# Kernel optimization log

Hardware: AMD Instinct MI355X
Metric: run time of the kernel (lower is better)

Reference implementation:

```python
import jax, jax.numpy as jnp
import numpy as np

ENC_VTH = 0.999      # ENCODER_REGULAR_VTH
CDECAY = 0.5         # NEURON_CDECAY
VDECAY = 0.75        # NEURON_VDECAY
VTH = 0.5            # NEURON_VTH
WIN = 0.5            # SPIKE_PSEUDO_GRAD_WINDOW
T = 5                # spike_ts

# --- pseudo-gradient spike functions ---
@jax.custom_vjp
def enc_spike(v):
    return (v > ENC_VTH).astype(v.dtype)
def _enc_fwd(v):
    return enc_spike(v), None
def _enc_bwd(_, g):
    return (g,)  # straight-through
enc_spike.defvjp(_enc_fwd, _enc_bwd)

@jax.custom_vjp
def rect_spike(v):
    return (v > VTH).astype(v.dtype)
def _rect_fwd(v):
    return rect_spike(v), v
def _rect_bwd(v, g):
    return (g * (jnp.abs(v - VTH) < WIN).astype(g.dtype),)
rect_spike.defvjp(_rect_fwd, _rect_bwd)


def setup_inputs() -> dict:
    key = jax.random.key(0)
    ks = jax.random.split(key, 8)
    B, obs_dim, en_pop, act_dim, de_pop = 8192, 128, 10, 8, 10
    H1, H2 = 256, 256
    N = obs_dim * en_pop           # 1280
    O = act_dim * de_pop           # 80
    obs = jax.random.normal(ks[0], (B, obs_dim), jnp.float32)
    # encoder mean: linspace over mean_range per population, std constant 0.15
    mean_row = jnp.linspace(-3.0, 3.0, en_pop, dtype=jnp.float32)
    enc_mean = jnp.broadcast_to(mean_row, (1, obs_dim, en_pop)).astype(jnp.float32)
    enc_std = jnp.full((1, obs_dim, en_pop), 0.15, jnp.float32)
    W1 = jax.random.normal(ks[1], (H1, N), jnp.float32) / np.sqrt(N)
    b1 = jnp.zeros((H1,), jnp.float32)
    W2 = jax.random.normal(ks[2], (H2, H1), jnp.float32) / np.sqrt(H1)
    b2 = jnp.zeros((H2,), jnp.float32)
    Wo = jax.random.normal(ks[3], (O, H2), jnp.float32) / np.sqrt(H2)
    bo = jnp.zeros((O,), jnp.float32)
    dec_w = jax.random.normal(ks[4], (act_dim, de_pop), jnp.float32) / np.sqrt(de_pop)
    dec_b = jnp.zeros((act_dim,), jnp.float32)
    log_std = jnp.full((act_dim,), -0.001, jnp.float32)
    return {"obs": obs, "enc_mean": enc_mean, "enc_std": enc_std,
            "W1": W1, "b1": b1, "W2": W2, "b2": b2, "Wo": Wo, "bo": bo,
            "dec_w": dec_w, "dec_b": dec_b, "log_std": log_std}


def reference(obs, enc_mean, enc_std, W1, b1, W2, b2, Wo, bo, dec_w, dec_b, log_std):
    B = obs.shape[0]
    # --- population encoder: gaussian receptive fields -> regular spike train ---
    pop_act = jnp.exp(-0.5 * (obs[:, :, None] - enc_mean) ** 2 / enc_std ** 2)
    pop_act = pop_act.reshape(B, -1)  # [B, obs_dim*en_pop]

    def enc_step(volt, _):
        volt = volt + pop_act
        s = enc_spike(volt)
        return volt - s * ENC_VTH, s
    _, spikes = jax.lax.scan(enc_step, jnp.zeros_like(pop_act), None, length=T)  # [T, B, N]

    # --- LIF neuron model ---
    def lif(x, W, b, c, v, s):
        c = c * CDECAY + x @ W.T + b
        v = v * VDECAY * (1.0 - s) + c
        s = rect_spike(v)
        return c, v, s

    H1, H2, O = W1.shape[0], W2.shape[0], Wo.shape[0]
    z = lambda n: jnp.zeros((B, n), dtype=obs.dtype)
    carry0 = ((z(H1), z(H1), z(H1)), (z(H2), z(H2), z(H2)), (z(O), z(O), z(O)), z(O))

    def snn_step(carry, x):
        (c1, v1, s1), (c2, v2, s2), (co, vo, so), acc = carry
        c1, v1, s1 = lif(x, W1, b1, c1, v1, s1)
        c2, v2, s2 = lif(s1, W2, b2, c2, v2, s2)
        co, vo, so = lif(s2, Wo, bo, co, vo, so)
        return ((c1, v1, s1), (c2, v2, s2), (co, vo, so), acc + so), None

    (_, _, _, acc), _ = jax.lax.scan(snn_step, carry0, spikes)
    out_pop_act = acc / T  # [B, act_dim*de_pop]

    # --- grouped Conv1d(kernel=de_pop, groups=act_dim) decoder + ELU ---
    act_dim, de_pop = dec_w.shape
    mu = jax.nn.elu(jnp.einsum('bap,ap->ba', out_pop_act.reshape(B, act_dim, de_pop), dec_w) + dec_b)
    std = jnp.exp(log_std)
    return mu, std
```

## Files before the change

kernel.cpp:

```cpp
#include <hip/hip_runtime.h>

typedef unsigned char  u8;
typedef unsigned short u16;
typedef unsigned int   u32;
typedef unsigned long long u64;
typedef __attribute__((ext_vector_type(8))) short bf16x8;
typedef __attribute__((ext_vector_type(4))) float f32x4;

#define NOBS 128
#define NN   1280
#define NH   256
#define NO   80
#define TT   5
#define RR   16
#define NTHR 512
#define BP1  88
#define BP2  20

#define W1TOT   983040
#define W2S_OFF 983040
#define WOS_OFF 1179648
#define WS_TOTAL 1277952

#define PREP_BLOCKS 4992

#define VMW2()  asm volatile("s_waitcnt vmcnt(2)" ::: "memory")
#define VMW0()  asm volatile("s_waitcnt vmcnt(0)" ::: "memory")
#define FENCE() asm volatile("" ::: "memory")

__device__ __forceinline__ float bf2f(u16 u) {
  union { u32 i; float f; } x; x.i = ((u32)u) << 16; return x.f;
}
__device__ __forceinline__ u16 f2bf(float f) {
  union { float f; u32 i; } x; x.f = f;
  u32 i = x.i + 0x7FFFu + ((x.i >> 16) & 1u);
  return (u16)(i >> 16);
}

__device__ __forceinline__ u16 split3(float w, int sel) {
  u16 hi = f2bf(w);
  if (sel == 0) return hi;
  float r1 = __fsub_rn(w, bf2f(hi));
  u16 mid = f2bf(r1);
  if (sel == 1) return mid;
  float r2 = __fsub_rn(r1, bf2f(mid));
  return f2bf(r2);
}

__device__ __forceinline__ float exp_cr(float arg) {
  double xa = (double)arg;
  double nd = __builtin_rint(xa * 1.4426950408889634074);
  double r  = fma(nd, -6.93147180369123816490e-01, xa);
  r         = fma(nd, -1.90821492927058770002e-10, r);
  double p = 2.50521083854417187751e-08;
  p = fma(p, r, 2.75573192239858906526e-07);
  p = fma(p, r, 2.75573192239858906526e-06);
  p = fma(p, r, 2.48015873015873015873e-05);
  p = fma(p, r, 1.98412698412698412698e-04);
  p = fma(p, r, 1.38888888888888888889e-03);
  p = fma(p, r, 8.33333333333333333333e-03);
  p = fma(p, r, 4.16666666666666666667e-02);
  p = fma(p, r, 1.66666666666666666667e-01);
  p = fma(p, r, 0.5);
  p = fma(p, r, 1.0);
  p = fma(p, r, 1.0);
  int n = (int)nd;
  union { u64 u; double d; } s;
  s.u = ((u64)(u32)(n + 1023)) << 52;
  return (n < -150) ? 0.f : (float)(s.d * p);
}

__global__ __launch_bounds__(256) void prep_w(
    const float* __restrict__ W1, const float* __restrict__ W2,
    const float* __restrict__ Wo, u16* __restrict__ ws)
{
  int i = blockIdx.x * 256 + threadIdx.x;
  if (i < W1TOT) {
    int kc = i / 49152, r = i - kc * 49152;
    int ks = r / 24576, r2 = r - ks * 24576;
    int sel = r2 / 8192, r3 = r2 & 8191;
    int j = r3 >> 5, kkpos = r3 & 31;
    int kk = ((kkpos >> 3) ^ ((j >> 1) & 3)) * 8 + (kkpos & 7);
    ws[i] = split3(W1[j * 1280 + kc * 64 + ks * 32 + kk], sel);
  } else if (i < WOS_OFF) {
    int i2 = i - W2S_OFF;
    int kc = i2 / 49152, r = i2 - kc * 49152;
    int ks = r / 24576, r2 = r - ks * 24576;
    int sel = r2 / 8192, r3 = r2 & 8191;
    int j = r3 >> 5, kkpos = r3 & 31;
    int kk = ((kkpos >> 3) ^ ((j >> 1) & 3)) * 8 + (kkpos & 7);
    ws[i] = split3(W2[j * 256 + kc * 64 + ks * 32 + kk], sel);
  } else {
    int i3 = i - WOS_OFF;
    int kc = i3 / 24576, r = i3 - kc * 24576;
    int ks = r / 12288, r2 = r - ks * 12288;
    int sel = r2 / 4096, r3 = r2 & 4095;
    int j = r3 >> 5, kkpos = r3 & 31;
    int kk = ((kkpos >> 3) ^ ((j >> 1) & 3)) * 8 + (kkpos & 7);
    float w = (j < NO) ? Wo[j * 256 + kc * 64 + ks * 32 + kk] : 0.f;
    ws[i] = split3(w, sel);
  }
}

__device__ __forceinline__ void dma2(const u16* __restrict__ src, u16* dst, int lane) {
  __builtin_amdgcn_global_load_lds((const u32*)(src + lane * 8), (u32*)dst, 16, 0, 0);
  __builtin_amdgcn_global_load_lds((const u32*)(src + 512 + lane * 8),
                                   (u32*)(dst + 512), 16, 0, 0);
}

__device__ __forceinline__ void gemm_wp(
    const u16* lbits, int bpitch,
    const u16* __restrict__ wsbase, int nkc, int selblk,
    u16* mybuf,
    int wv, int lane, f32x4 acc[2][TT])
{
  const int m16 = lane & 15, q = lane >> 4;
  const int swz = (q ^ ((m16 >> 1) & 3)) * 8;
  const int lro0 = m16 * 32 + swz;
  const int lro1 = lro0 + 512;
  const int sh = q * 8;
  const int nst = nkc * 6;
  const u16* slice = wsbase + wv * 1024;

  dma2(slice, mybuf, lane);
  dma2(slice + selblk, mybuf + 1024, lane);
  FENCE();
  VMW2();
  bf16x8 cur0 = *(const bf16x8*)(mybuf + lro0);
  bf16x8 cur1 = *(const bf16x8*)(mybuf + lro1);
  FENCE();

  int st = 0;
  for (int kcks = 0; kcks < nkc * 2; ++kcks) {
    const int kc = kcks >> 1, ks = kcks & 1;
    bf16x8 afr[TT];
    #pragma unroll
    for (int t = 0; t < TT; ++t) {
      u32 bwv = *(const u32*)(lbits + (t * RR + m16) * bpitch + kc * 4 + ks * 2);
      u32 b = (bwv >> sh) & 0xFFu;
      union { u32 u[4]; bf16x8 v; } x;
      #pragma unroll
      for (int i = 0; i < 4; ++i)
        x.u[i] = ((((b >> (2 * i)) & 3u) * 0x8001u) & 0x00010001u) * 0x3F80u;
      afr[t] = x.v;
    }
    #pragma unroll
    for (int sel = 0; sel < 3; ++sel, ++st) {
      if (st + 2 < nst)
        dma2(slice + (st + 2) * selblk, mybuf + ((sel + 2) % 3) * 1024, lane);
      FENCE();
      #pragma unroll
      for (int t = 0; t < TT; ++t)
        acc[0][t] = __builtin_amdgcn_mfma_f32_16x16x32_bf16(afr[t], cur0, acc[0][t], 0, 0, 0);
      #pragma unroll
      for (int t = 0; t < TT; ++t)
        acc[1][t] = __builtin_amdgcn_mfma_f32_16x16x32_bf16(afr[t], cur1, acc[1][t], 0, 0, 0);
      if (st + 1 < nst) {
        if (st + 2 < nst) { VMW2(); } else { VMW0(); }
        const u16* nb = mybuf + ((sel + 1) % 3) * 1024;
        cur0 = *(const bf16x8*)(nb + lro0);
        cur1 = *(const bf16x8*)(nb + lro1);
      }
      FENCE();
    }
  }
}

__device__ __forceinline__ void recur_spikes2(
    f32x4 acc[2][TT], const float* __restrict__ bias,
    int lane, int wv, u16* sbits, int spitch)
{
  const int q = lane >> 4, m16 = lane & 15;
  #pragma unroll
  for (int i = 0; i < 2; ++i) {
    int ct = wv * 2 + i;
    int j = ct * 16 + m16;
    float bj = bias[j];
    #pragma unroll
    for (int rg = 0; rg < 4; ++rg) {
      float c = 0.f, v = 0.f, sprev = 0.f;
      #pragma unroll
      for (int t = 0; t < TT; ++t) {
        float u = acc[i][t][rg];
        c = __fadd_rn(__fadd_rn(__fmul_rn(c, 0.5f), u), bj);
        float vd = __fmul_rn(v, 0.75f);
        v = __fadd_rn((sprev > 0.5f) ? 0.f : vd, c);
        bool sp = v > 0.5f;
        u64 mask = __ballot(sp);
        if (m16 == 0) {
          int row = q * 4 + rg;
          sbits[(t * RR + row) * spitch + ct] = (u16)(mask >> (q * 16));
        }
        sprev = sp ? 1.f : 0.f;
      }
    }
  }
}

__global__ __launch_bounds__(NTHR, 4) void snn_main(
    const float* __restrict__ obs, const float* __restrict__ enc_mean,
    const float* __restrict__ enc_std,
    const float* __restrict__ b1, const float* __restrict__ b2, const float* __restrict__ bo,
    const float* __restrict__ dec_w, const float* __restrict__ dec_b, const float* __restrict__ log_std,
    const u16* __restrict__ wsW, float* __restrict__ out, int Btot)
{
  __shared__ __align__(16) u16 smem[37376];
  u16* bufs = smem;
  u16* encb = smem + 24576;
  u16* s1b  = encb + 7040;
  u16* s2b  = s1b + 1600;
  float* soacc = (float*)(s2b + 1600);

  const int tid  = threadIdx.x;
  const int lane = tid & 63;
  const int wv   = tid >> 6;
  const int r0   = blockIdx.x * RR;
  u16* mybuf = bufs + wv * 3072;

  for (int h = tid; h < RR * 160; h += NTHR) {
    int r = h / 160, rem = h - r * 160;
    int w = rem >> 1, hi = rem & 1;
    const float* obsrow = obs + (r0 + r) * NOBS;
    u32 bits[TT] = {0, 0, 0, 0, 0};
    #pragma unroll
    for (int e = 0; e < 8; ++e) {
      int k = w * 16 + hi * 8 + e;
      int f = k / 10;
      float x  = obsrow[f];
      float m  = enc_mean[k];
      float sd = enc_std[k];
      float d  = __fsub_rn(x, m);
      float arg = __fdiv_rn(__fmul_rn(-0.5f, __fmul_rn(d, d)), __fmul_rn(sd, sd));
      float a = exp_cr(arg);
      float v = 0.f;
      #pragma unroll
      for (int t = 0; t < TT; ++t) {
        v = __fadd_rn(v, a);
        if (v > 0.999f) { bits[t] |= (1u << e); v = __fsub_rn(v, 0.999f); }
      }
    }
    u8* eb = (u8*)encb;
    #pragma unroll
    for (int t = 0; t < TT; ++t)
      eb[((t * RR + r) * BP1 + w) * 2 + hi] = (u8)bits[t];
  }
  __syncthreads();

  f32x4 acc[2][TT];
  const f32x4 zero4 = {0.f, 0.f, 0.f, 0.f};
#define ZERO_ACC() { _Pragma("unroll") for (int i = 0; i < 2; ++i) \
                     _Pragma("unroll") for (int t = 0; t < TT; ++t) acc[i][t] = zero4; }

  ZERO_ACC();
  gemm_wp(encb, BP1, wsW, 20, 8192, mybuf, wv, lane, acc);
  recur_spikes2(acc, b1, lane, wv, s1b, BP2);
  __syncthreads();

  ZERO_ACC();
  gemm_wp(s1b, BP2, wsW + W2S_OFF, 4, 8192, mybuf, wv, lane, acc);
  recur_spikes2(acc, b2, lane, wv, s2b, BP2);
  __syncthreads();

  if (wv < 3) {
    ZERO_ACC();
    gemm_wp(s2b, BP2, wsW + WOS_OFF, 4, 4096, mybuf, wv, lane, acc);
    const int q = lane >> 4, m16 = lane & 15;
    #pragma unroll
    for (int i = 0; i < 2; ++i) {
      int j = (wv * 2 + i) * 16 + m16;
      bool valid = j < NO;
      float bj = valid ? bo[j] : 0.f;
      #pragma unroll
      for (int rg = 0; rg < 4; ++rg) {
        float c = 0.f, v = 0.f, sprev = 0.f;
        int cnt = 0;
        #pragma unroll
        for (int t = 0; t < TT; ++t) {
          float u = acc[i][t][rg];
          c = __fadd_rn(__fadd_rn(__fmul_rn(c, 0.5f), u), bj);
          float vd = __fmul_rn(v, 0.75f);
          v = __fadd_rn((sprev > 0.5f) ? 0.f : vd, c);
          bool sp = v > 0.5f;
          cnt += sp ? 1 : 0;
          sprev = sp ? 1.f : 0.f;
        }
        if (valid) soacc[(q * 4 + rg) * NO + j] = __fdiv_rn((float)cnt, 5.0f);
      }
    }
  }
  __syncthreads();

  if (tid < RR * 8) {
    int r = tid >> 3, a = tid & 7;
    float s = 0.f;
    const float* so = soacc + r * NO + a * 10;
    #pragma unroll
    for (int p = 0; p < 10; ++p)
      s = __fadd_rn(s, __fmul_rn(so[p], dec_w[a * 10 + p]));
    s = __fadd_rn(s, dec_b[a]);
    float mu = (s > 0.f) ? s : expm1f(s);
    out[(r0 + r) * 8 + a] = mu;
  }
  if (blockIdx.x == 0 && tid < 8) {
    out[Btot * 8 + tid] = expf(log_std[tid]);
  }
}

extern "C" void kernel_launch(void* const* d_in, const int* in_sizes, int n_in,
                              void* d_out, int out_size, void* d_ws, size_t ws_size,
                              hipStream_t stream) {
  const float* obs      = (const float*)d_in[0];
  const float* enc_mean = (const float*)d_in[1];
  const float* enc_std  = (const float*)d_in[2];
  const float* W1       = (const float*)d_in[3];
  const float* b1       = (const float*)d_in[4];
  const float* W2       = (const float*)d_in[5];
  const float* b2       = (const float*)d_in[6];
  const float* Wo       = (const float*)d_in[7];
  const float* bo       = (const float*)d_in[8];
  const float* dec_w    = (const float*)d_in[9];
  const float* dec_b    = (const float*)d_in[10];
  const float* log_std  = (const float*)d_in[11];
  u16*   ws  = (u16*)d_ws;
  float* out = (float*)d_out;
  int B = in_sizes[0] / NOBS;

  hipLaunchKernelGGL(prep_w, dim3(PREP_BLOCKS), dim3(256), 0, stream,
                     W1, W2, Wo, ws);
  hipLaunchKernelGGL(snn_main, dim3(B / RR), dim3(NTHR), 0, stream,
                     obs, enc_mean, enc_std, b1, b2, bo, dec_w, dec_b, log_std,
                     ws, out, B);
}
```

Before: 178.0 us.

## Vectorize weight prep, use LDS LUT for spike fragments, strength-reduce DMA addresses

The weight-prep kernel now has each thread load 8 consecutive floats and write hi/mid/lo bf16 splits as 16-byte stores, which cuts the prep grid from 4992 to 208 blocks and removes per-element index math and redundant loads. In the main kernel, spike-bit-to-bf16 fragment expansion uses a 16-entry u64 lookup table in shared memory instead of per-element multiply/mask arithmetic. DMA source addresses are precomputed per lane and incremented rather than recomputed. The LUT adds LDS reads on the hot loop and a small shared-memory increase. The LUT is filled by threads 0-15 before the encoder loop, and the __syncthreads that follows the encoder loop orders it before its first use in gemm_wp.

```diff
diff --git a/kernel.cpp b/kernel.cpp
--- a/kernel.cpp
+++ b/kernel.cpp
@@ -22,7 +22,7 @@
 #define WOS_OFF 1179648
 #define WS_TOTAL 1277952
 
-#define PREP_BLOCKS 4992
+#define PREP_BLOCKS 208
 
 #define VMW2()  asm volatile("s_waitcnt vmcnt(2)" ::: "memory")
 #define VMW0()  asm volatile("s_waitcnt vmcnt(0)" ::: "memory")
@@ -35,16 +35,6 @@
   union { float f; u32 i; } x; x.f = f;
   u32 i = x.i + 0x7FFFu + ((x.i >> 16) & 1u);
   return (u16)(i >> 16);
-}
-
-__device__ __forceinline__ u16 split3(float w, int sel) {
-  u16 hi = f2bf(w);
-  if (sel == 0) return hi;
-  float r1 = __fsub_rn(w, bf2f(hi));
-  u16 mid = f2bf(r1);
-  if (sel == 1) return mid;
-  float r2 = __fsub_rn(r1, bf2f(mid));
-  return f2bf(r2);
 }
 
 __device__ __forceinline__ float exp_cr(float arg) {
@@ -74,44 +64,69 @@
     const float* __restrict__ W1, const float* __restrict__ W2,
     const float* __restrict__ Wo, u16* __restrict__ ws)
 {
-  int i = blockIdx.x * 256 + threadIdx.x;
-  if (i < W1TOT) {
-    int kc = i / 49152, r = i - kc * 49152;
-    int ks = r / 24576, r2 = r - ks * 24576;
-    int sel = r2 / 8192, r3 = r2 & 8191;
-    int j = r3 >> 5, kkpos = r3 & 31;
-    int kk = ((kkpos >> 3) ^ ((j >> 1) & 3)) * 8 + (kkpos & 7);
-    ws[i] = split3(W1[j * 1280 + kc * 64 + ks * 32 + kk], sel);
-  } else if (i < WOS_OFF) {
-    int i2 = i - W2S_OFF;
-    int kc = i2 / 49152, r = i2 - kc * 49152;
-    int ks = r / 24576, r2 = r - ks * 24576;
-    int sel = r2 / 8192, r3 = r2 & 8191;
-    int j = r3 >> 5, kkpos = r3 & 31;
-    int kk = ((kkpos >> 3) ^ ((j >> 1) & 3)) * 8 + (kkpos & 7);
-    ws[i] = split3(W2[j * 256 + kc * 64 + ks * 32 + kk], sel);
+  const int T = blockIdx.x * 256 + threadIdx.x;
+  const float* src;
+  int dstb, selstep;
+  bool pad = false;
+  if (T < 40960) {
+    int kcks = T >> 10, r = T & 1023;
+    int kc = kcks >> 1, ks = kcks & 1, j = r >> 2, kgrp = r & 3;
+    int kk0 = (kgrp ^ ((j >> 1) & 3)) << 3;
+    src = W1 + j * 1280 + kc * 64 + ks * 32 + kk0;
+    dstb = kc * 49152 + ks * 24576 + j * 32 + kgrp * 8;
+    selstep = 8192;
+  } else if (T < 49152) {
+    int T2 = T - 40960;
+    int kcks = T2 >> 10, r = T2 & 1023;
+    int kc = kcks >> 1, ks = kcks & 1, j = r >> 2, kgrp = r & 3;
+    int kk0 = (kgrp ^ ((j >> 1) & 3)) << 3;
+    src = W2 + j * 256 + kc * 64 + ks * 32 + kk0;
+    dstb = W2S_OFF + kc * 49152 + ks * 24576 + j * 32 + kgrp * 8;
+    selstep = 8192;
   } else {
-    int i3 = i - WOS_OFF;
-    int kc = i3 / 24576, r = i3 - kc * 24576;
-    int ks = r / 12288, r2 = r - ks * 12288;
-    int sel = r2 / 4096, r3 = r2 & 4095;
-    int j = r3 >> 5, kkpos = r3 & 31;
-    int kk = ((kkpos >> 3) ^ ((j >> 1) & 3)) * 8 + (kkpos & 7);
-    float w = (j < NO) ? Wo[j * 256 + kc * 64 + ks * 32 + kk] : 0.f;
-    ws[i] = split3(w, sel);
-  }
-}
-
-__device__ __forceinline__ void dma2(const u16* __restrict__ src, u16* dst, int lane) {
-  __builtin_amdgcn_global_load_lds((const u32*)(src + lane * 8), (u32*)dst, 16, 0, 0);
-  __builtin_amdgcn_global_load_lds((const u32*)(src + 512 + lane * 8),
+    int T3 = T - 49152;
+    int kcks = T3 >> 9, r = T3 & 511;
+    int kc = kcks >> 1, ks = kcks & 1, j = r >> 2, kgrp = r & 3;
+    int kk0 = (kgrp ^ ((j >> 1) & 3)) << 3;
+    src = Wo + j * 256 + kc * 64 + ks * 32 + kk0;
+    dstb = WOS_OFF + kc * 24576 + ks * 12288 + j * 32 + kgrp * 8;
+    selstep = 4096;
+    pad = (j >= NO);
+  }
+  float w[8];
+  if (!pad) {
+    float4 w0 = *(const float4*)src;
+    float4 w1 = *(const float4*)(src + 4);
+    w[0] = w0.x; w[1] = w0.y; w[2] = w0.z; w[3] = w0.w;
+    w[4] = w1.x; w[5] = w1.y; w[6] = w1.z; w[7] = w1.w;
+  } else {
+    #pragma unroll
+    for (int e = 0; e < 8; ++e) w[e] = 0.f;
+  }
+  union { u16 u[8]; uint4 q; } hi, mid, lo;
+  #pragma unroll
+  for (int e = 0; e < 8; ++e) {
+    u16 h = f2bf(w[e]);
+    float r1 = __fsub_rn(w[e], bf2f(h));
+    u16 m = f2bf(r1);
+    float r2 = __fsub_rn(r1, bf2f(m));
+    hi.u[e] = h; mid.u[e] = m; lo.u[e] = f2bf(r2);
+  }
+  *(uint4*)(ws + dstb)               = hi.q;
+  *(uint4*)(ws + dstb + selstep)     = mid.q;
+  *(uint4*)(ws + dstb + 2 * selstep) = lo.q;
+}
+
+__device__ __forceinline__ void dma2(const u16* __restrict__ lane_src, u16* dst) {
+  __builtin_amdgcn_global_load_lds((const u32*)lane_src, (u32*)dst, 16, 0, 0);
+  __builtin_amdgcn_global_load_lds((const u32*)(lane_src + 512),
                                    (u32*)(dst + 512), 16, 0, 0);
 }
 
 __device__ __forceinline__ void gemm_wp(
     const u16* lbits, int bpitch,
     const u16* __restrict__ wsbase, int nkc, int selblk,
-    u16* mybuf,
+    u16* mybuf, const u64* __restrict__ lut,
     int wv, int lane, f32x4 acc[2][TT])
 {
   const int m16 = lane & 15, q = lane >> 4;
@@ -120,10 +135,11 @@
   const int lro1 = lro0 + 512;
   const int sh = q * 8;
   const int nst = nkc * 6;
-  const u16* slice = wsbase + wv * 1024;
-
-  dma2(slice, mybuf, lane);
-  dma2(slice + selblk, mybuf + 1024, lane);
+  const u16* lsrc = wsbase + wv * 1024 + lane * 8;
+
+  dma2(lsrc, mybuf);
+  dma2(lsrc + selblk, mybuf + 1024);
+  const u16* nsrc = lsrc + 2 * selblk;
   FENCE();
   VMW2();
   bf16x8 cur0 = *(const bf16x8*)(mybuf + lro0);
@@ -138,16 +154,17 @@
     for (int t = 0; t < TT; ++t) {
       u32 bwv = *(const u32*)(lbits + (t * RR + m16) * bpitch + kc * 4 + ks * 2);
       u32 b = (bwv >> sh) & 0xFFu;
-      union { u32 u[4]; bf16x8 v; } x;
-      #pragma unroll
-      for (int i = 0; i < 4; ++i)
-        x.u[i] = ((((b >> (2 * i)) & 3u) * 0x8001u) & 0x00010001u) * 0x3F80u;
+      union { u64 d[2]; bf16x8 v; } x;
+      x.d[0] = lut[b & 15u];
+      x.d[1] = lut[b >> 4];
       afr[t] = x.v;
     }
     #pragma unroll
     for (int sel = 0; sel < 3; ++sel, ++st) {
-      if (st + 2 < nst)
-        dma2(slice + (st + 2) * selblk, mybuf + ((sel + 2) % 3) * 1024, lane);
+      if (st + 2 < nst) {
+        dma2(nsrc, mybuf + ((sel + 2) % 3) * 1024);
+        nsrc += selblk;
+      }
       FENCE();
       #pragma unroll
       for (int t = 0; t < TT; ++t)
@@ -204,18 +221,25 @@
     const float* __restrict__ dec_w, const float* __restrict__ dec_b, const float* __restrict__ log_std,
     const u16* __restrict__ wsW, float* __restrict__ out, int Btot)
 {
-  __shared__ __align__(16) u16 smem[37376];
+  __shared__ __align__(16) u16 smem[37440];
   u16* bufs = smem;
   u16* encb = smem + 24576;
   u16* s1b  = encb + 7040;
   u16* s2b  = s1b + 1600;
   float* soacc = (float*)(s2b + 1600);
+  u64* lutp = (u64*)(smem + 37376);
 
   const int tid  = threadIdx.x;
   const int lane = tid & 63;
   const int wv   = tid >> 6;
   const int r0   = blockIdx.x * RR;
   u16* mybuf = bufs + wv * 3072;
+
+  if (tid < 16) {
+    u32 lo32 = (((tid & 3u) * 0x8001u) & 0x10001u) * 0x3F80u;
+    u32 hi32 = ((((tid >> 2) & 3u) * 0x8001u) & 0x10001u) * 0x3F80u;
+    lutp[tid] = (u64)lo32 | ((u64)hi32 << 32);
+  }
 
   for (int h = tid; h < RR * 160; h += NTHR) {
     int r = h / 160, rem = h - r * 160;
@@ -252,18 +276,18 @@
                      _Pragma("unroll") for (int t = 0; t < TT; ++t) acc[i][t] = zero4; }
 
   ZERO_ACC();
-  gemm_wp(encb, BP1, wsW, 20, 8192, mybuf, wv, lane, acc);
+  gemm_wp(encb, BP1, wsW, 20, 8192, mybuf, lutp, wv, lane, acc);
   recur_spikes2(acc, b1, lane, wv, s1b, BP2);
   __syncthreads();
 
   ZERO_ACC();
-  gemm_wp(s1b, BP2, wsW + W2S_OFF, 4, 8192, mybuf, wv, lane, acc);
+  gemm_wp(s1b, BP2, wsW + W2S_OFF, 4, 8192, mybuf, lutp, wv, lane, acc);
   recur_spikes2(acc, b2, lane, wv, s2b, BP2);
   __syncthreads();
 
   if (wv < 3) {
     ZERO_ACC();
-    gemm_wp(s2b, BP2, wsW + WOS_OFF, 4, 4096, mybuf, wv, lane, acc);
+    gemm_wp(s2b, BP2, wsW + WOS_OFF, 4, 4096, mybuf, lutp, wv, lane, acc);
     const int q = lane >> 4, m16 = lane & 15;
     #pragma unroll
     for (int i = 0; i < 2; ++i) {
```

After: 167.9 us. 1.06x faster.
